# Kernel tuning notes

Measured on AMD Instinct MI355X. Metric: run time of the kernel, lower is better.

The kernel has to match this reference:

```python
import jax, jax.numpy as jnp
import numpy as np

N_NODES = 500_000
N_EDGES = 16_000_000
D = 2


def setup_inputs() -> dict:
    key = jax.random.key(0)
    k_x, k_e = jax.random.split(key)
    x = jax.random.normal(k_x, (N_NODES, D), dtype=jnp.float32)
    edge_index = jax.random.randint(k_e, (2, N_EDGES), 0, N_NODES, dtype=jnp.int32)
    # Weights exactly as loaded in the module's state_dict
    W_rel = jnp.eye(D, dtype=jnp.float32)   # lin_rel.weight
    b_rel = jnp.zeros((D,), dtype=jnp.float32)  # lin_rel.bias
    W_root = jnp.eye(D, dtype=jnp.float32)  # lin_root.weight (no bias)
    return {"x": x, "edge_index": edge_index, "W_rel": W_rel, "b_rel": b_rel, "W_root": W_root}


def reference(x, edge_index, W_rel, b_rel, W_root):
    # PyG GraphConv(aggr='add'):
    #   out = lin_rel( sum_{j in N(i)} x_j ) + lin_root(x_i)
    src, dst = edge_index[0], edge_index[1]
    # gather neighbor features along edges, scatter-add into destination nodes
    aggr = jax.ops.segment_sum(x[src], dst, num_segments=N_NODES)  # [N, D]
    out = aggr @ W_rel.T + b_rel + x @ W_root.T
    return out
```

## Files before the change

### kernel.cpp

```cpp
#include <hip/hip_runtime.h>

#define NPB       2048
#define NB_SHIFT  11
#define NBUCKETS  245
#define CAP1      81920
#define P1S_THREADS 1024
#define EPT1S     16
#define P2I_THREADS 1024
#define P2_UNROLL 8
#define FXSCALE   1048576.0f
#define FXINV     (1.0f / 1048576.0f)
#define EPT       32
#define P1_THREADS 256
#define P2_THREADS 1024

typedef unsigned int uint4_ev  __attribute__((ext_vector_type(4)));
typedef float        float4_ev __attribute__((ext_vector_type(4)));
typedef int          int4_ev   __attribute__((ext_vector_type(4)));
typedef int          int2_ev   __attribute__((ext_vector_type(2)));

#define OFF_CUR1  0ULL
#define OFF_XI    4096ULL
#define SZ_XI     (512ULL * 2048 * 8)
#define OFF_RECS  (OFF_XI + SZ_XI)
#define SZ_RECS   (245ULL * CAP1 * 4)
#define OFF_END   (OFF_RECS + SZ_RECS)


__global__ __launch_bounds__(256)
void xconv(const float* __restrict__ xf, int* __restrict__ xi, int n_nodes) {
    int i = blockIdx.x * 256 + threadIdx.x;
    int base = i * 4;
    if (base >= NBUCKETS * NPB * 2) return;
    float4_ev v = {0.f, 0.f, 0.f, 0.f};
    if (base + 3 < n_nodes * 2) {
        v = *reinterpret_cast<const float4_ev*>(xf + base);
    } else {
        for (int j = 0; j < 4; ++j)
            if (base + j < n_nodes * 2) { ((float*)&v)[j] = xf[base + j]; }
    }
    int4_ev iv;
    iv.x = __float2int_rn(v.x * FXSCALE);
    iv.y = __float2int_rn(v.y * FXSCALE);
    iv.z = __float2int_rn(v.z * FXSCALE);
    iv.w = __float2int_rn(v.w * FXSCALE);
    *reinterpret_cast<int4_ev*>(xi + base) = iv;
}

__global__ __launch_bounds__(P1S_THREADS)
void p1s_bucket(const int* __restrict__ src,
                const int* __restrict__ dst,
                int* __restrict__ cursors,
                unsigned int* __restrict__ recs,
                int n_edges) {
    __shared__ unsigned sorted[P1S_THREADS * EPT1S];
    __shared__ int hist[NBUCKETS], startl[NBUCKETS], lofs[NBUCKETS], gbase[NBUCKETS];
    const int tid = threadIdx.x;
    if (tid < NBUCKETS) { hist[tid] = 0; lofs[tid] = 0; }
    __syncthreads();

    const int blockBase = blockIdx.x * (P1S_THREADS * EPT1S);
    int m = n_edges - blockBase;
    if (m > P1S_THREADS * EPT1S) m = P1S_THREADS * EPT1S;

    int s[EPT1S], d[EPT1S];
#pragma unroll
    for (int k = 0; k < EPT1S / 4; ++k) {
        int e = k * (P1S_THREADS * 4) + tid * 4;
        if (e + 3 < m) {
            int4 s4 = *reinterpret_cast<const int4*>(src + blockBase + e);
            int4 d4 = *reinterpret_cast<const int4*>(dst + blockBase + e);
            s[4*k] = s4.x; s[4*k+1] = s4.y; s[4*k+2] = s4.z; s[4*k+3] = s4.w;
            d[4*k] = d4.x; d[4*k+1] = d4.y; d[4*k+2] = d4.z; d[4*k+3] = d4.w;
        } else {
#pragma unroll
            for (int j = 0; j < 4; ++j) {
                int ee = e + j;
                if (ee < m) { s[4*k+j] = src[blockBase + ee]; d[4*k+j] = dst[blockBase + ee]; }
                else        { s[4*k+j] = 0;                   d[4*k+j] = -1;                  }
            }
        }
    }

#pragma unroll
    for (int j = 0; j < EPT1S; ++j)
        if (d[j] >= 0) atomicAdd(&hist[d[j] >> NB_SHIFT], 1);
    __syncthreads();

    if (tid < 64) {
        int carry = 0;
        for (int c = 0; c < (NBUCKETS + 63) / 64; ++c) {
            int i = c * 64 + tid;
            int v = (i < NBUCKETS) ? hist[i] : 0;
            int sacc = v;
#pragma unroll
            for (int dsh = 1; dsh < 64; dsh <<= 1) {
                int t = __shfl_up(sacc, dsh);
                if (tid >= dsh) sacc += t;
            }
            if (i < NBUCKETS) startl[i] = carry + sacc - v;
            carry += __shfl(sacc, 63);
        }
    }
    if (tid < NBUCKETS) {
        int c = hist[tid];
        gbase[tid] = (c > 0) ? atomicAdd(&cursors[tid], c) : 0;
    }
    __syncthreads();

#pragma unroll
    for (int j = 0; j < EPT1S; ++j) {
        if (d[j] >= 0) {
            int bk = d[j] >> NB_SHIFT;
            int p = startl[bk] + atomicAdd(&lofs[bk], 1);
            sorted[p] = ((unsigned)s[j] << NB_SHIFT) | (unsigned)(d[j] & (NPB - 1));
        }
    }
    __syncthreads();

    const int wave = tid >> 6, lane = tid & 63;
    for (int b = wave; b < NBUCKETS; b += (P1S_THREADS / 64)) {
        int s0 = startl[b];
        int c  = hist[b];
        int gb = gbase[b];
        int cmax = CAP1 - gb; if (cmax < 0) cmax = 0;
        if (c > cmax) c = cmax;
        unsigned int* dp = recs + (size_t)b * CAP1 + gb;
        for (int i = lane; i < c; i += 64) dp[i] = sorted[s0 + i];
    }
}

__global__ __launch_bounds__(P2I_THREADS)
void p2i_reduce(const unsigned int* __restrict__ recs,
                const int* __restrict__ cursors,
                const int2_ev* __restrict__ xi,
                const float2* __restrict__ x,
                const float* __restrict__ W_rel,
                const float* __restrict__ b_rel,
                const float* __restrict__ W_root,
                float2* __restrict__ out,
                int n_nodes) {
    __shared__ int acc[NPB * 2];
    const int bk = blockIdx.x;
    const int tid = threadIdx.x;
    for (int i = tid; i < NPB * 2; i += P2I_THREADS) acc[i] = 0;
    __syncthreads();

    int cnt = cursors[bk];
    if (cnt > CAP1) cnt = CAP1;
    const unsigned int* r = recs + (size_t)bk * CAP1;

    const int ngroups = cnt / P2_UNROLL;
    for (int g = tid; g < ngroups; g += P2I_THREADS) {
        const uint4_ev* p0 = reinterpret_cast<const uint4_ev*>(r + g * P2_UNROLL);
        uint4_ev a = __builtin_nontemporal_load(p0);
        uint4_ev b = __builtin_nontemporal_load(p0 + 1);
        unsigned rec[P2_UNROLL] = {a.x, a.y, a.z, a.w, b.x, b.y, b.z, b.w};
        int2_ev v[P2_UNROLL];
#pragma unroll
        for (int k = 0; k < P2_UNROLL; ++k)
            v[k] = xi[rec[k] >> NB_SHIFT];
#pragma unroll
        for (int k = 0; k < P2_UNROLL; ++k) {
            int loc = rec[k] & (NPB - 1);
            atomicAdd(&acc[loc * 2],     v[k].x);
            atomicAdd(&acc[loc * 2 + 1], v[k].y);
        }
    }
    for (int i = ngroups * P2_UNROLL + tid; i < cnt; i += P2I_THREADS) {
        unsigned rec = r[i];
        int2_ev v = xi[rec >> NB_SHIFT];
        int loc = rec & (NPB - 1);
        atomicAdd(&acc[loc * 2],     v.x);
        atomicAdd(&acc[loc * 2 + 1], v.y);
    }
    __syncthreads();

    const float w00 = W_rel[0],  w01 = W_rel[1],  w10 = W_rel[2],  w11 = W_rel[3];
    const float r00 = W_root[0], r01 = W_root[1], r10 = W_root[2], r11 = W_root[3];
    const float b0 = b_rel[0], b1 = b_rel[1];
    const int node0 = bk * NPB;
    for (int i = tid; i < NPB; i += P2I_THREADS) {
        int node = node0 + i;
        if (node < n_nodes) {
            float2 xv = x[node];
            float a0 = (float)acc[i * 2]     * FXINV;
            float a1 = (float)acc[i * 2 + 1] * FXINV;
            float2 o;
            o.x = b0 + w00 * a0 + w01 * a1 + r00 * xv.x + r01 * xv.y;
            o.y = b1 + w10 * a0 + w11 * a1 + r10 * xv.x + r11 * xv.y;
            out[node] = o;
        }
    }
}


__global__ __launch_bounds__(P1_THREADS)
void p1_bucket(const int* __restrict__ src,
               const int* __restrict__ dst,
               int* __restrict__ cursors,
               unsigned int* __restrict__ recs,
               int cap, int n_edges) {
    __shared__ int hist[NBUCKETS];
    __shared__ int base[NBUCKETS];
    __shared__ int lofs[NBUCKETS];
    const int tid = threadIdx.x;
    for (int i = tid; i < NBUCKETS; i += P1_THREADS) { hist[i] = 0; lofs[i] = 0; }
    __syncthreads();

    const int blockBase = blockIdx.x * (P1_THREADS * EPT);
    int s[EPT], d[EPT];

#pragma unroll
    for (int k = 0; k < EPT / 4; ++k) {
        int e = blockBase + k * (P1_THREADS * 4) + tid * 4;
        if (e + 3 < n_edges) {
            int4 s4 = *reinterpret_cast<const int4*>(src + e);
            int4 d4 = *reinterpret_cast<const int4*>(dst + e);
            s[4*k] = s4.x; s[4*k+1] = s4.y; s[4*k+2] = s4.z; s[4*k+3] = s4.w;
            d[4*k] = d4.x; d[4*k+1] = d4.y; d[4*k+2] = d4.z; d[4*k+3] = d4.w;
        } else {
#pragma unroll
            for (int j = 0; j < 4; ++j) {
                int ee = e + j;
                if (ee < n_edges) { s[4*k+j] = src[ee]; d[4*k+j] = dst[ee]; }
                else              { s[4*k+j] = 0;       d[4*k+j] = -1;      }
            }
        }
    }

#pragma unroll
    for (int j = 0; j < EPT; ++j)
        if (d[j] >= 0) atomicAdd(&hist[d[j] >> NB_SHIFT], 1);
    __syncthreads();

    for (int i = tid; i < NBUCKETS; i += P1_THREADS) {
        int c = hist[i];
        base[i] = (c > 0) ? atomicAdd(&cursors[i], c) : 0;
    }
    __syncthreads();

#pragma unroll
    for (int j = 0; j < EPT; ++j) {
        if (d[j] >= 0) {
            int bk = d[j] >> NB_SHIFT;
            int p = base[bk] + atomicAdd(&lofs[bk], 1);
            if (p < cap)
                recs[(size_t)bk * cap + p] =
                    ((unsigned)s[j] << NB_SHIFT) | (unsigned)(d[j] & (NPB - 1));
        }
    }
}

__global__ __launch_bounds__(P2_THREADS)
void p2_reduce(const unsigned int* __restrict__ recs,
               const int* __restrict__ cursors,
               const float2* __restrict__ x,
               const float* __restrict__ W_rel,
               const float* __restrict__ b_rel,
               const float* __restrict__ W_root,
               float2* __restrict__ out,
               int cap, int n_nodes) {
    __shared__ float acc[NPB * 2];
    const int bk = blockIdx.x;
    const int tid = threadIdx.x;
    for (int i = tid; i < NPB * 2; i += P2_THREADS) acc[i] = 0.0f;
    __syncthreads();

    int cnt = cursors[bk];
    if (cnt > cap) cnt = cap;
    const unsigned int* r = recs + (size_t)bk * cap;

    const int ngroups = cnt / P2_UNROLL;
    for (int g = tid; g < ngroups; g += P2_THREADS) {
        const uint4_ev* p0 = reinterpret_cast<const uint4_ev*>(r + g * P2_UNROLL);
        uint4_ev a = __builtin_nontemporal_load(p0);
        uint4_ev b = __builtin_nontemporal_load(p0 + 1);
        unsigned rec[P2_UNROLL] = {a.x, a.y, a.z, a.w, b.x, b.y, b.z, b.w};
        float2 xv[P2_UNROLL];
#pragma unroll
        for (int k = 0; k < P2_UNROLL; ++k)
            xv[k] = x[rec[k] >> NB_SHIFT];
#pragma unroll
        for (int k = 0; k < P2_UNROLL; ++k) {
            int loc = rec[k] & (NPB - 1);
            atomicAdd(&acc[loc * 2],     xv[k].x);
            atomicAdd(&acc[loc * 2 + 1], xv[k].y);
        }
    }
    for (int i = ngroups * P2_UNROLL + tid; i < cnt; i += P2_THREADS) {
        unsigned rec = r[i];
        float2 xv = x[rec >> NB_SHIFT];
        int loc = rec & (NPB - 1);
        atomicAdd(&acc[loc * 2],     xv.x);
        atomicAdd(&acc[loc * 2 + 1], xv.y);
    }
    __syncthreads();

    const float w00 = W_rel[0],  w01 = W_rel[1],  w10 = W_rel[2],  w11 = W_rel[3];
    const float r00 = W_root[0], r01 = W_root[1], r10 = W_root[2], r11 = W_root[3];
    const float b0 = b_rel[0], b1 = b_rel[1];
    const int node0 = bk * NPB;
    for (int i = tid; i < NPB; i += P2_THREADS) {
        int node = node0 + i;
        if (node < n_nodes) {
            float2 xv = x[node];
            float a0 = acc[i * 2], a1 = acc[i * 2 + 1];
            float2 o;
            o.x = b0 + w00 * a0 + w01 * a1 + r00 * xv.x + r01 * xv.y;
            o.y = b1 + w10 * a0 + w11 * a1 + r10 * xv.x + r11 * xv.y;
            out[node] = o;
        }
    }
}


__global__ void init_out_kernel(const float2* __restrict__ x,
                                const float* __restrict__ W_root,
                                const float* __restrict__ b_rel,
                                float2* __restrict__ out, int n) {
    int i = blockIdx.x * blockDim.x + threadIdx.x;
    const float w00 = W_root[0], w01 = W_root[1], w10 = W_root[2], w11 = W_root[3];
    const float b0 = b_rel[0], b1 = b_rel[1];
    if (i < n) {
        float2 xv = x[i];
        float2 o;
        o.x = b0 + w00 * xv.x + w01 * xv.y;
        o.y = b1 + w10 * xv.x + w11 * xv.y;
        out[i] = o;
    }
}

__global__ void edge_scatter_kernel(const int* __restrict__ src,
                                    const int* __restrict__ dst,
                                    const float2* __restrict__ x,
                                    const float* __restrict__ W_rel,
                                    float* __restrict__ out, int n_edges) {
    const float w00 = W_rel[0], w01 = W_rel[1], w10 = W_rel[2], w11 = W_rel[3];
    int base = (blockIdx.x * blockDim.x + threadIdx.x) * 4;
    if (base + 3 < n_edges) {
        int4 s4 = *reinterpret_cast<const int4*>(src + base);
        int4 d4 = *reinterpret_cast<const int4*>(dst + base);
        int ss[4] = {s4.x, s4.y, s4.z, s4.w};
        int dd[4] = {d4.x, d4.y, d4.z, d4.w};
#pragma unroll
        for (int k = 0; k < 4; ++k) {
            float2 xv = x[ss[k]];
            unsafeAtomicAdd(&out[2 * dd[k]],     w00 * xv.x + w01 * xv.y);
            unsafeAtomicAdd(&out[2 * dd[k] + 1], w10 * xv.x + w11 * xv.y);
        }
    } else {
        for (int e = base; e < n_edges; ++e) {
            int s = src[e], d = dst[e];
            float2 xv = x[s];
            unsafeAtomicAdd(&out[2 * d],     w00 * xv.x + w01 * xv.y);
            unsafeAtomicAdd(&out[2 * d + 1], w10 * xv.x + w11 * xv.y);
        }
    }
}


extern "C" void kernel_launch(void* const* d_in, const int* in_sizes, int n_in,
                              void* d_out, int out_size, void* d_ws, size_t ws_size,
                              hipStream_t stream) {
    const float* x        = (const float*)d_in[0];
    const int*   edge_idx = (const int*)d_in[1];
    const float* W_rel    = (const float*)d_in[2];
    const float* b_rel    = (const float*)d_in[3];
    const float* W_root   = (const float*)d_in[4];
    float* out = (float*)d_out;

    const int n_nodes = in_sizes[0] / 2;
    const int n_edges = in_sizes[1] / 2;
    const int* src = edge_idx;
    const int* dst = edge_idx + n_edges;

    const bool shape_ok = (n_nodes <= NBUCKETS * NPB) && (n_nodes < (1 << 19));

    if (shape_ok && ws_size >= OFF_END) {
        int* curs1 = (int*)((char*)d_ws + OFF_CUR1);
        int* xi    = (int*)((char*)d_ws + OFF_XI);
        unsigned int* recs = (unsigned int*)((char*)d_ws + OFF_RECS);

        (void)hipMemsetAsync(d_ws, 0, 4096, stream);

        int xc_blocks = (NBUCKETS * NPB * 2 / 4 + 255) / 256;
        xconv<<<xc_blocks, 256, 0, stream>>>(x, xi, n_nodes);

        int p1_blocks = (n_edges + P1S_THREADS * EPT1S - 1) / (P1S_THREADS * EPT1S);
        p1s_bucket<<<p1_blocks, P1S_THREADS, 0, stream>>>(
            src, dst, curs1, recs, n_edges);

        p2i_reduce<<<NBUCKETS, P2I_THREADS, 0, stream>>>(
            recs, curs1, (const int2_ev*)xi, (const float2*)x,
            W_rel, b_rel, W_root, (float2*)out, n_nodes);
        return;
    }

    const size_t rec_off = 4096;
    long long cap = 0;
    if (ws_size > rec_off)
        cap = (long long)((ws_size - rec_off) / sizeof(unsigned int)) / NBUCKETS;
    if (cap > 131072) cap = 131072;

    if (shape_ok && cap >= 67584) {
        int* cursors = (int*)d_ws;
        unsigned int* recs = (unsigned int*)((char*)d_ws + rec_off);

        (void)hipMemsetAsync(cursors, 0, NBUCKETS * sizeof(int), stream);

        int p1_blocks = (n_edges + P1_THREADS * EPT - 1) / (P1_THREADS * EPT);
        p1_bucket<<<p1_blocks, P1_THREADS, 0, stream>>>(
            src, dst, cursors, recs, (int)cap, n_edges);

        p2_reduce<<<NBUCKETS, P2_THREADS, 0, stream>>>(
            recs, cursors, (const float2*)x, W_rel, b_rel, W_root,
            (float2*)out, (int)cap, n_nodes);
    } else {
        {
            int threads = 256;
            int blocks = (n_nodes + threads - 1) / threads;
            init_out_kernel<<<blocks, threads, 0, stream>>>(
                (const float2*)x, W_root, b_rel, (float2*)out, n_nodes);
        }
        {
            int threads = 256;
            int epb = threads * 4;
            int blocks = (n_edges + epb - 1) / epb;
            edge_scatter_kernel<<<blocks, threads, 0, stream>>>(
                src, dst, (const float2*)x, W_rel, out, n_edges);
        }
    }
}
```

Before: 151.4 us.

## Split per-bucket reduction across two blocks, merge partials, pad cursors

The per-bucket reduce kernel now launches two blocks per bucket, each handling half of the bucket's records and writing an integer partial accumulator to workspace. A new merge kernel then sums the two partials and applies the linear layers. Bucket cursors are padded to a 16-int stride to avoid atomic contention on shared cache lines, and the bucketing kernel's block size drops from 1024 to 512. This aims to fill more CUs than 245 blocks could, at the cost of an extra kernel launch and roughly 8 MB of extra partial-buffer traffic.

```diff
diff --git a/kernel.cpp b/kernel.cpp
--- a/kernel.cpp
+++ b/kernel.cpp
@@ -4,10 +4,13 @@
 #define NB_SHIFT  11
 #define NBUCKETS  245
 #define CAP1      81920
-#define P1S_THREADS 1024
+#define CURS_STRIDE 16
+#define P1S_THREADS 512
 #define EPT1S     16
 #define P2I_THREADS 1024
+#define SPLIT2    2
 #define P2_UNROLL 8
+#define PM_THREADS 256
 #define FXSCALE   1048576.0f
 #define FXINV     (1.0f / 1048576.0f)
 #define EPT       32
@@ -19,10 +22,12 @@
 typedef int          int4_ev   __attribute__((ext_vector_type(4)));
 typedef int          int2_ev   __attribute__((ext_vector_type(2)));
 
-#define OFF_CUR1  0ULL
-#define OFF_XI    4096ULL
+#define OFF_CURS  0ULL
+#define OFF_XI    16384ULL
 #define SZ_XI     (512ULL * 2048 * 8)
-#define OFF_RECS  (OFF_XI + SZ_XI)
+#define OFF_PART  (OFF_XI + SZ_XI)
+#define SZ_PART   (245ULL * SPLIT2 * NPB * 2 * 4)
+#define OFF_RECS  (OFF_PART + SZ_PART)
 #define SZ_RECS   (245ULL * CAP1 * 4)
 #define OFF_END   (OFF_RECS + SZ_RECS)
 
@@ -104,7 +109,7 @@
     }
     if (tid < NBUCKETS) {
         int c = hist[tid];
-        gbase[tid] = (c > 0) ? atomicAdd(&cursors[tid], c) : 0;
+        gbase[tid] = (c > 0) ? atomicAdd(&cursors[tid * CURS_STRIDE], c) : 0;
     }
     __syncthreads();
 
@@ -131,67 +136,83 @@
 }
 
 __global__ __launch_bounds__(P2I_THREADS)
-void p2i_reduce(const unsigned int* __restrict__ recs,
-                const int* __restrict__ cursors,
-                const int2_ev* __restrict__ xi,
-                const float2* __restrict__ x,
-                const float* __restrict__ W_rel,
-                const float* __restrict__ b_rel,
-                const float* __restrict__ W_root,
-                float2* __restrict__ out,
-                int n_nodes) {
+void p2i_partial(const unsigned int* __restrict__ recs,
+                 const int* __restrict__ cursors,
+                 const int2_ev* __restrict__ xi,
+                 int* __restrict__ partials) {
     __shared__ int acc[NPB * 2];
-    const int bk = blockIdx.x;
+    const int bk = blockIdx.x >> 1;
+    const int sb = blockIdx.x & 1;
     const int tid = threadIdx.x;
     for (int i = tid; i < NPB * 2; i += P2I_THREADS) acc[i] = 0;
     __syncthreads();
 
-    int cnt = cursors[bk];
+    int cnt = cursors[bk * CURS_STRIDE];
     if (cnt > CAP1) cnt = CAP1;
-    const unsigned int* r = recs + (size_t)bk * CAP1;
-
-    const int ngroups = cnt / P2_UNROLL;
-    for (int g = tid; g < ngroups; g += P2I_THREADS) {
-        const uint4_ev* p0 = reinterpret_cast<const uint4_ev*>(r + g * P2_UNROLL);
-        uint4_ev a = __builtin_nontemporal_load(p0);
-        uint4_ev b = __builtin_nontemporal_load(p0 + 1);
-        unsigned rec[P2_UNROLL] = {a.x, a.y, a.z, a.w, b.x, b.y, b.z, b.w};
-        int2_ev v[P2_UNROLL];
-#pragma unroll
-        for (int k = 0; k < P2_UNROLL; ++k)
-            v[k] = xi[rec[k] >> NB_SHIFT];
-#pragma unroll
-        for (int k = 0; k < P2_UNROLL; ++k) {
-            int loc = rec[k] & (NPB - 1);
-            atomicAdd(&acc[loc * 2],     v[k].x);
-            atomicAdd(&acc[loc * 2 + 1], v[k].y);
-        }
-    }
-    for (int i = ngroups * P2_UNROLL + tid; i < cnt; i += P2I_THREADS) {
-        unsigned rec = r[i];
-        int2_ev v = xi[rec >> NB_SHIFT];
-        int loc = rec & (NPB - 1);
-        atomicAdd(&acc[loc * 2],     v.x);
-        atomicAdd(&acc[loc * 2 + 1], v.y);
-    }
-    __syncthreads();
-
+    int chunk = (((cnt + 1) >> 1) + 7) & ~7;
+    int lo = sb * chunk;
+    int hi = lo + chunk; if (hi > cnt) hi = cnt;
+    int m = hi - lo;
+
+    if (m > 0) {
+        const unsigned int* r = recs + (size_t)bk * CAP1 + lo;
+        const int ngroups = m / P2_UNROLL;
+        for (int g = tid; g < ngroups; g += P2I_THREADS) {
+            const uint4_ev* p0 = reinterpret_cast<const uint4_ev*>(r + g * P2_UNROLL);
+            uint4_ev a = __builtin_nontemporal_load(p0);
+            uint4_ev b = __builtin_nontemporal_load(p0 + 1);
+            unsigned rec[P2_UNROLL] = {a.x, a.y, a.z, a.w, b.x, b.y, b.z, b.w};
+            int2_ev v[P2_UNROLL];
+#pragma unroll
+            for (int k = 0; k < P2_UNROLL; ++k)
+                v[k] = xi[rec[k] >> NB_SHIFT];
+#pragma unroll
+            for (int k = 0; k < P2_UNROLL; ++k) {
+                int loc = rec[k] & (NPB - 1);
+                atomicAdd(&acc[loc * 2],     v[k].x);
+                atomicAdd(&acc[loc * 2 + 1], v[k].y);
+            }
+        }
+        for (int i = ngroups * P2_UNROLL + tid; i < m; i += P2I_THREADS) {
+            unsigned rec = r[i];
+            int2_ev v = xi[rec >> NB_SHIFT];
+            int loc = rec & (NPB - 1);
+            atomicAdd(&acc[loc * 2],     v.x);
+            atomicAdd(&acc[loc * 2 + 1], v.y);
+        }
+    }
+    __syncthreads();
+
+    int* pp = partials + (size_t)blockIdx.x * (NPB * 2);
+    for (int i = tid * 4; i < NPB * 2; i += P2I_THREADS * 4)
+        *reinterpret_cast<int4_ev*>(pp + i) =
+            *reinterpret_cast<const int4_ev*>(&acc[i]);
+}
+
+__global__ __launch_bounds__(PM_THREADS)
+void pmerge(const int* __restrict__ partials,
+            const float2* __restrict__ x,
+            const float* __restrict__ W_rel,
+            const float* __restrict__ b_rel,
+            const float* __restrict__ W_root,
+            float2* __restrict__ out,
+            int n_nodes) {
+    int i = blockIdx.x * PM_THREADS + threadIdx.x;
+    if (i >= n_nodes) return;
+    const int bk  = i >> NB_SHIFT;
+    const int loc = i & (NPB - 1);
+    const int* p0 = partials + (size_t)(bk * SPLIT2) * (NPB * 2) + loc * 2;
+    const int* p1 = p0 + NPB * 2;
+    float a0 = (float)(p0[0] + p1[0]) * FXINV;
+    float a1 = (float)(p0[1] + p1[1]) * FXINV;
     const float w00 = W_rel[0],  w01 = W_rel[1],  w10 = W_rel[2],  w11 = W_rel[3];
     const float r00 = W_root[0], r01 = W_root[1], r10 = W_root[2], r11 = W_root[3];
     const float b0 = b_rel[0], b1 = b_rel[1];
-    const int node0 = bk * NPB;
-    for (int i = tid; i < NPB; i += P2I_THREADS) {
-        int node = node0 + i;
-        if (node < n_nodes) {
-            float2 xv = x[node];
-            float a0 = (float)acc[i * 2]     * FXINV;
-            float a1 = (float)acc[i * 2 + 1] * FXINV;
-            float2 o;
-            o.x = b0 + w00 * a0 + w01 * a1 + r00 * xv.x + r01 * xv.y;
-            o.y = b1 + w10 * a0 + w11 * a1 + r10 * xv.x + r11 * xv.y;
-            out[node] = o;
-        }
-    }
+    float2 xv = x[i];
+    float2 o;
+    o.x = b0 + w00 * a0 + w01 * a1 + r00 * xv.x + r01 * xv.y;
+    o.y = b1 + w10 * a0 + w11 * a1 + r10 * xv.x + r11 * xv.y;
+    out[i] = o;
 }
 
 
@@ -378,22 +399,27 @@
     const bool shape_ok = (n_nodes <= NBUCKETS * NPB) && (n_nodes < (1 << 19));
 
     if (shape_ok && ws_size >= OFF_END) {
-        int* curs1 = (int*)((char*)d_ws + OFF_CUR1);
-        int* xi    = (int*)((char*)d_ws + OFF_XI);
+        int* cursors = (int*)((char*)d_ws + OFF_CURS);
+        int* xi      = (int*)((char*)d_ws + OFF_XI);
+        int* partials = (int*)((char*)d_ws + OFF_PART);
         unsigned int* recs = (unsigned int*)((char*)d_ws + OFF_RECS);
 
-        (void)hipMemsetAsync(d_ws, 0, 4096, stream);
+        (void)hipMemsetAsync(d_ws, 0, 16384, stream);
 
         int xc_blocks = (NBUCKETS * NPB * 2 / 4 + 255) / 256;
         xconv<<<xc_blocks, 256, 0, stream>>>(x, xi, n_nodes);
 
         int p1_blocks = (n_edges + P1S_THREADS * EPT1S - 1) / (P1S_THREADS * EPT1S);
         p1s_bucket<<<p1_blocks, P1S_THREADS, 0, stream>>>(
-            src, dst, curs1, recs, n_edges);
-
-        p2i_reduce<<<NBUCKETS, P2I_THREADS, 0, stream>>>(
-            recs, curs1, (const int2_ev*)xi, (const float2*)x,
-            W_rel, b_rel, W_root, (float2*)out, n_nodes);
+            src, dst, cursors, recs, n_edges);
+
+        p2i_partial<<<NBUCKETS * SPLIT2, P2I_THREADS, 0, stream>>>(
+            recs, cursors, (const int2_ev*)xi, partials);
+
+        int pm_blocks = (n_nodes + PM_THREADS - 1) / PM_THREADS;
+        pmerge<<<pm_blocks, PM_THREADS, 0, stream>>>(
+            partials, (const float2*)x, W_rel, b_rel, W_root,
+            (float2*)out, n_nodes);
         return;
     }
 
```

After: 165.8 us (median of 2 runs). 1.09x slower.

## Pack both feature components into one 64-bit biased fixed-point word for single LDS atomic

Applied to the files above, without the earlier changes.

Each node's two features are quantized to biased 27-bit fixed-point fields with a count field in the top bits, so one 64-bit shared-memory atomic replaces two 32-bit atomics per edge. The reduce kernel decodes the sums by subtracting count times the bias. Cursor counters are also padded to separate cache lines so bucket atomics from different blocks do not share a line. This trades precision: the fixed-point scale drops from 2^20 to 2^15 and inputs are clamped, and the 27-bit fields can overflow if a node's in-degree times the bias gets too large.

```diff
diff --git a/kernel.cpp b/kernel.cpp
--- a/kernel.cpp
+++ b/kernel.cpp
@@ -4,47 +4,43 @@
 #define NB_SHIFT  11
 #define NBUCKETS  245
 #define CAP1      81920
+#define CURS_STRIDE 16
 #define P1S_THREADS 1024
 #define EPT1S     16
 #define P2I_THREADS 1024
 #define P2_UNROLL 8
-#define FXSCALE   1048576.0f
-#define FXINV     (1.0f / 1048576.0f)
+#define PK_SCALE  32768.0f
+#define PK_INV    (1.0f / 32768.0f)
+#define PK_BIAS   262144
+#define PK_MASK   ((1u << 27) - 1)
 #define EPT       32
 #define P1_THREADS 256
 #define P2_THREADS 1024
 
 typedef unsigned int uint4_ev  __attribute__((ext_vector_type(4)));
 typedef float        float4_ev __attribute__((ext_vector_type(4)));
-typedef int          int4_ev   __attribute__((ext_vector_type(4)));
-typedef int          int2_ev   __attribute__((ext_vector_type(2)));
-
-#define OFF_CUR1  0ULL
-#define OFF_XI    4096ULL
-#define SZ_XI     (512ULL * 2048 * 8)
-#define OFF_RECS  (OFF_XI + SZ_XI)
+typedef unsigned long long ull;
+
+#define OFF_CURS  0ULL
+#define OFF_XP    16384ULL
+#define SZ_XP     (512ULL * 2048 * 8)
+#define OFF_RECS  (OFF_XP + SZ_XP)
 #define SZ_RECS   (245ULL * CAP1 * 4)
 #define OFF_END   (OFF_RECS + SZ_RECS)
 
 
 __global__ __launch_bounds__(256)
-void xconv(const float* __restrict__ xf, int* __restrict__ xi, int n_nodes) {
+void xconv(const float2* __restrict__ xf, ull* __restrict__ xp, int n_nodes) {
     int i = blockIdx.x * 256 + threadIdx.x;
-    int base = i * 4;
-    if (base >= NBUCKETS * NPB * 2) return;
-    float4_ev v = {0.f, 0.f, 0.f, 0.f};
-    if (base + 3 < n_nodes * 2) {
-        v = *reinterpret_cast<const float4_ev*>(xf + base);
-    } else {
-        for (int j = 0; j < 4; ++j)
-            if (base + j < n_nodes * 2) { ((float*)&v)[j] = xf[base + j]; }
-    }
-    int4_ev iv;
-    iv.x = __float2int_rn(v.x * FXSCALE);
-    iv.y = __float2int_rn(v.y * FXSCALE);
-    iv.z = __float2int_rn(v.z * FXSCALE);
-    iv.w = __float2int_rn(v.w * FXSCALE);
-    *reinterpret_cast<int4_ev*>(xi + base) = iv;
+    if (i >= NBUCKETS * NPB) return;
+    float2 v = (i < n_nodes) ? xf[i] : make_float2(0.f, 0.f);
+    int xq = __float2int_rn(v.x * PK_SCALE);
+    int yq = __float2int_rn(v.y * PK_SCALE);
+    xq = min(max(xq, -PK_BIAS + 1), PK_BIAS - 1);
+    yq = min(max(yq, -PK_BIAS + 1), PK_BIAS - 1);
+    xp[i] = (1ULL << 54) |
+            ((ull)(unsigned)(yq + PK_BIAS) << 27) |
+            (ull)(unsigned)(xq + PK_BIAS);
 }
 
 __global__ __launch_bounds__(P1S_THREADS)
@@ -104,7 +100,7 @@
     }
     if (tid < NBUCKETS) {
         int c = hist[tid];
-        gbase[tid] = (c > 0) ? atomicAdd(&cursors[tid], c) : 0;
+        gbase[tid] = (c > 0) ? atomicAdd(&cursors[tid * CURS_STRIDE], c) : 0;
     }
     __syncthreads();
 
@@ -131,22 +127,22 @@
 }
 
 __global__ __launch_bounds__(P2I_THREADS)
-void p2i_reduce(const unsigned int* __restrict__ recs,
+void p2p_reduce(const unsigned int* __restrict__ recs,
                 const int* __restrict__ cursors,
-                const int2_ev* __restrict__ xi,
+                const ull* __restrict__ xp,
                 const float2* __restrict__ x,
                 const float* __restrict__ W_rel,
                 const float* __restrict__ b_rel,
                 const float* __restrict__ W_root,
                 float2* __restrict__ out,
                 int n_nodes) {
-    __shared__ int acc[NPB * 2];
+    __shared__ ull acc[NPB];
     const int bk = blockIdx.x;
     const int tid = threadIdx.x;
-    for (int i = tid; i < NPB * 2; i += P2I_THREADS) acc[i] = 0;
-    __syncthreads();
-
-    int cnt = cursors[bk];
+    for (int i = tid; i < NPB; i += P2I_THREADS) acc[i] = 0ULL;
+    __syncthreads();
+
+    int cnt = cursors[bk * CURS_STRIDE];
     if (cnt > CAP1) cnt = CAP1;
     const unsigned int* r = recs + (size_t)bk * CAP1;
 
@@ -156,23 +152,17 @@
         uint4_ev a = __builtin_nontemporal_load(p0);
         uint4_ev b = __builtin_nontemporal_load(p0 + 1);
         unsigned rec[P2_UNROLL] = {a.x, a.y, a.z, a.w, b.x, b.y, b.z, b.w};
-        int2_ev v[P2_UNROLL];
+        ull v[P2_UNROLL];
 #pragma unroll
         for (int k = 0; k < P2_UNROLL; ++k)
-            v[k] = xi[rec[k] >> NB_SHIFT];
-#pragma unroll
-        for (int k = 0; k < P2_UNROLL; ++k) {
-            int loc = rec[k] & (NPB - 1);
-            atomicAdd(&acc[loc * 2],     v[k].x);
-            atomicAdd(&acc[loc * 2 + 1], v[k].y);
-        }
+            v[k] = xp[rec[k] >> NB_SHIFT];
+#pragma unroll
+        for (int k = 0; k < P2_UNROLL; ++k)
+            atomicAdd(&acc[rec[k] & (NPB - 1)], v[k]);
     }
     for (int i = ngroups * P2_UNROLL + tid; i < cnt; i += P2I_THREADS) {
         unsigned rec = r[i];
-        int2_ev v = xi[rec >> NB_SHIFT];
-        int loc = rec & (NPB - 1);
-        atomicAdd(&acc[loc * 2],     v.x);
-        atomicAdd(&acc[loc * 2 + 1], v.y);
+        atomicAdd(&acc[rec & (NPB - 1)], xp[rec >> NB_SHIFT]);
     }
     __syncthreads();
 
@@ -183,9 +173,13 @@
     for (int i = tid; i < NPB; i += P2I_THREADS) {
         int node = node0 + i;
         if (node < n_nodes) {
+            ull w = acc[i];
+            int n  = (int)(w >> 54);
+            int xs = (int)((unsigned)(w        & PK_MASK)) - n * PK_BIAS;
+            int ys = (int)((unsigned)((w >> 27) & PK_MASK)) - n * PK_BIAS;
+            float a0 = (float)xs * PK_INV;
+            float a1 = (float)ys * PK_INV;
             float2 xv = x[node];
-            float a0 = (float)acc[i * 2]     * FXINV;
-            float a1 = (float)acc[i * 2 + 1] * FXINV;
             float2 o;
             o.x = b0 + w00 * a0 + w01 * a1 + r00 * xv.x + r01 * xv.y;
             o.y = b1 + w10 * a0 + w11 * a1 + r10 * xv.x + r11 * xv.y;
@@ -378,21 +372,21 @@
     const bool shape_ok = (n_nodes <= NBUCKETS * NPB) && (n_nodes < (1 << 19));
 
     if (shape_ok && ws_size >= OFF_END) {
-        int* curs1 = (int*)((char*)d_ws + OFF_CUR1);
-        int* xi    = (int*)((char*)d_ws + OFF_XI);
+        int* cursors = (int*)((char*)d_ws + OFF_CURS);
+        ull* xp      = (ull*)((char*)d_ws + OFF_XP);
         unsigned int* recs = (unsigned int*)((char*)d_ws + OFF_RECS);
 
-        (void)hipMemsetAsync(d_ws, 0, 4096, stream);
-
-        int xc_blocks = (NBUCKETS * NPB * 2 / 4 + 255) / 256;
-        xconv<<<xc_blocks, 256, 0, stream>>>(x, xi, n_nodes);
+        (void)hipMemsetAsync(d_ws, 0, 16384, stream);
+
+        int xc_blocks = (NBUCKETS * NPB + 255) / 256;
+        xconv<<<xc_blocks, 256, 0, stream>>>((const float2*)x, xp, n_nodes);
 
         int p1_blocks = (n_edges + P1S_THREADS * EPT1S - 1) / (P1S_THREADS * EPT1S);
         p1s_bucket<<<p1_blocks, P1S_THREADS, 0, stream>>>(
-            src, dst, curs1, recs, n_edges);
-
-        p2i_reduce<<<NBUCKETS, P2I_THREADS, 0, stream>>>(
-            recs, curs1, (const int2_ev*)xi, (const float2*)x,
+            src, dst, cursors, recs, n_edges);
+
+        p2p_reduce<<<NBUCKETS, P2I_THREADS, 0, stream>>>(
+            recs, cursors, xp, (const float2*)x,
             W_rel, b_rel, W_root, (float2*)out, n_nodes);
         return;
     }
```

After: 155.3 us. +2.6%, slower.
